# Optimization experiments

Measured on AMD Instinct MI355X. Metric: run time of the kernel, lower is better.

## Reference

```python
import jax, jax.numpy as jnp
import numpy as np
import math

B, S, D_MODEL, H = 4, 256, 2048, 256
HEAD_DIM = D_MODEL // H  # 8


def setup_inputs() -> dict:
    key = jax.random.key(0)
    ks = jax.random.split(key, 10)
    w_scale = 0.02
    inp = {
        "x": jax.random.normal(ks[0], (B, S, D_MODEL), dtype=jnp.float32),
        "phase_shift": jax.random.normal(ks[1], (H, 1, 1), dtype=jnp.float32),
        "Wq": jax.random.normal(ks[2], (D_MODEL, D_MODEL), dtype=jnp.float32) * w_scale,
        "bq": jnp.zeros((D_MODEL,), dtype=jnp.float32),
        "Wk": jax.random.normal(ks[3], (D_MODEL, D_MODEL), dtype=jnp.float32) * w_scale,
        "bk": jnp.zeros((D_MODEL,), dtype=jnp.float32),
        "Wv": jax.random.normal(ks[4], (D_MODEL, D_MODEL), dtype=jnp.float32) * w_scale,
        "bv": jnp.zeros((D_MODEL,), dtype=jnp.float32),
        "Wo": jax.random.normal(ks[5], (D_MODEL, D_MODEL), dtype=jnp.float32) * w_scale,
        "bo": jnp.zeros((D_MODEL,), dtype=jnp.float32),
    }
    return inp


def _forward(x, phase_shift, Wq, bq, Wk, bk, Wv, bv, Wo, bo):
    b, s, dm = x.shape
    h = phase_shift.shape[0]
    d = dm // h
    # projections (torch Linear with random weights; stored as [in,out])
    q = (x @ Wq + bq).reshape(b, s, h, d)
    k = (x @ Wk + bk).reshape(b, s, h, d)
    v = (x @ Wv + bv).reshape(b, s, h, d)
    # complex phase rotation: q *= exp(+i phi), k *= exp(-i phi)
    # phase_shift (h,1,1) broadcasts against (b,s,h,d) -> varies along the s dim (requires s==h)
    c = jnp.cos(phase_shift)  # (h,1,1)
    sn = jnp.sin(phase_shift)
    qr, qi = q * c, q * sn          # Re/Im of rotated q
    kr, ki = k * c, -(k * sn)       # Re/Im of rotated k
    scale = 1.0 / math.sqrt(d)
    # per-(b,s) head-mixing scores: [b,s,h,h], complex matmul split into real/imag
    sr = (jnp.einsum('bshd,bsgd->bshg', qr, kr)
          - jnp.einsum('bshd,bsgd->bshg', qi, ki)) * scale
    si = (jnp.einsum('bshd,bsgd->bshg', qr, ki)
          + jnp.einsum('bshd,bsgd->bshg', qi, kr)) * scale  # analytically 0 (phases cancel)
    attn_r = jax.nn.softmax(sr, axis=-1)
    attn_i = jax.nn.softmax(si, axis=-1)  # faithful dual softmax; v is real so only
    # Re(attention @ v) = attn_r @ v reaches the output (.real is taken before o_proj)
    del attn_i
    out = jnp.einsum('bshg,bsgd->bshd', attn_r, v).reshape(b, s, dm)
    return out @ Wo + bo


def reference(x, phase_shift, Wq, bq, Wk, bk, Wv, bv, Wo, bo):
    return _forward(x, phase_shift, Wq, bq, Wk, bk, Wv, bv, Wo, bo)
```

## Files before the change

### kernel.cpp

```cpp
#include <hip/hip_runtime.h>
#include <math.h>

#define M_TOK 1024
#define DM    2048
#define NH    256
#define HD    8
#define SCALE 0.35355339059327373f
#define LOG2E 1.4426950408889634f

typedef _Float16 f16x8 __attribute__((ext_vector_type(8)));
typedef _Float16 f16x4 __attribute__((ext_vector_type(4)));
typedef float    f32x4 __attribute__((ext_vector_type(4)));

#if defined(__has_builtin)
#  if __has_builtin(__builtin_amdgcn_exp2f)
#    define EXP2(x) __builtin_amdgcn_exp2f(x)
#  endif
#endif
#ifndef EXP2
#  define EXP2(x) exp2f(x)
#endif

template<int N>
__device__ __forceinline__ void vm_wait() {
    if constexpr (N == 0) asm volatile("s_waitcnt vmcnt(0)" ::: "memory");
    else if constexpr (N == 1) asm volatile("s_waitcnt vmcnt(1)" ::: "memory");
    else if constexpr (N == 2) asm volatile("s_waitcnt vmcnt(2)" ::: "memory");
    else if constexpr (N == 3) asm volatile("s_waitcnt vmcnt(3)" ::: "memory");
    else if constexpr (N == 4) asm volatile("s_waitcnt vmcnt(4)" ::: "memory");
    else if constexpr (N == 5) asm volatile("s_waitcnt vmcnt(5)" ::: "memory");
    else if constexpr (N == 6) asm volatile("s_waitcnt vmcnt(6)" ::: "memory");
    else if constexpr (N == 7) asm volatile("s_waitcnt vmcnt(7)" ::: "memory");
    else if constexpr (N == 8) asm volatile("s_waitcnt vmcnt(8)" ::: "memory");
    else static_assert(N <= 8, "add vmcnt case");
}

__device__ __forceinline__ void raw_barrier() {
    asm volatile("" ::: "memory");
    __builtin_amdgcn_s_barrier();
    asm volatile("" ::: "memory");
}

__global__ __launch_bounds__(256) void prep(
    const float* __restrict__ x, _Float16* __restrict__ xh,
    const float* __restrict__ W0, const float* __restrict__ W1,
    const float* __restrict__ W2, const float* __restrict__ W3,
    _Float16* __restrict__ T0, _Float16* __restrict__ T1,
    _Float16* __restrict__ T2, _Float16* __restrict__ T3)
{
    __shared__ float t[64][65];
    const int tid = threadIdx.x;
    const int z   = blockIdx.z;

    if (z == 4) {
        const int i = (blockIdx.y * 32 + blockIdx.x) * 256 + tid;
        const float4 a = ((const float4*)x)[2 * i];
        const float4 b = ((const float4*)x)[2 * i + 1];
        f16x8 v;
        v[0] = (_Float16)a.x; v[1] = (_Float16)a.y; v[2] = (_Float16)a.z; v[3] = (_Float16)a.w;
        v[4] = (_Float16)b.x; v[5] = (_Float16)b.y; v[6] = (_Float16)b.z; v[7] = (_Float16)b.w;
        ((f16x8*)xh)[i] = v;
        return;
    }

    const float* W = (z == 0) ? W0 : (z == 1) ? W1 : (z == 2) ? W2 : W3;
    _Float16*    T = (z == 0) ? T0 : (z == 1) ? T1 : (z == 2) ? T2 : T3;

    const int nb = blockIdx.x * 64;
    const int kb = blockIdx.y * 64;
    const int tr = tid >> 4;
    const int tc = (tid & 15) << 2;

    #pragma unroll
    for (int rr = 0; rr < 4; ++rr) {
        const int k = kb + rr * 16 + tr;
        const float4 v = *(const float4*)&W[(size_t)k * DM + nb + tc];
        t[rr * 16 + tr][tc + 0] = v.x;
        t[rr * 16 + tr][tc + 1] = v.y;
        t[rr * 16 + tr][tc + 2] = v.z;
        t[rr * 16 + tr][tc + 3] = v.w;
    }
    __syncthreads();
    #pragma unroll
    for (int rr = 0; rr < 4; ++rr) {
        const int n = nb + rr * 16 + tr;
        f16x4 v;
        #pragma unroll
        for (int j = 0; j < 4; ++j)
            v[j] = (_Float16)t[tc + j][rr * 16 + tr];
        *(f16x4*)&T[(size_t)n * DM + kb + tc] = v;
    }
}

template<int WGR, int WGC, int WTR, int WTC, bool F16OUT, int MINW, int CS>
__global__ __launch_bounds__(256, MINW) void gemm_db(
    const _Float16* __restrict__ A,
    const _Float16* __restrict__ Bt,
    const float* __restrict__ b0, const float* __restrict__ b1,
    const float* __restrict__ b2, void* __restrict__ C)
{
    constexpr int BM  = WGR * WTR * 16;
    constexpr int BN  = WGC * WTC * 16;
    constexpr int NA  = BM / 8;
    constexpr int NB  = BN / 8;
    constexpr int NC  = NA + NB;
    constexpr int CPW = NC / 4;
    static_assert(NC % 4 == 0);
    constexpr int BUF = (BM + BN) * 64;

    __shared__ _Float16 smem[2 * BUF];

    const int bn = blockIdx.x * BN;
    const int bm = blockIdx.y * BM;

    const int tid  = threadIdx.x;
    const int lane = tid & 63;
    const int wv   = tid >> 6;
    const int wr   = (wv / WGC) * (WTR * 16);
    const int wc   = (wv % WGC) * (WTC * 16);
    const int lr   = lane & 15;
    const int lk   = lane >> 4;
    const int rx   = lr & 7;

    const _Float16* gsrc[CPW];
    int             loff[CPW];
    #pragma unroll
    for (int p = 0; p < CPW; ++p) {
        const int c   = wv * CPW + p;
        const int kch = ((lane & 7) ^ (lane >> 3)) << 3;
        if (c < NA) {
            const int rl = c * 8 + (lane >> 3);
            gsrc[p] = A + (size_t)(bm + rl) * DM + kch;
            loff[p] = c * 512 + lane * 8;
        } else {
            const int rl = (c - NA) * 8 + (lane >> 3);
            gsrc[p] = Bt + (size_t)(bn + rl) * DM + kch;
            loff[p] = BM * 64 + (c - NA) * 512 + lane * 8;
        }
    }

    int offA[WTR][2], offB[WTC][2];
    #pragma unroll
    for (int ks = 0; ks < 2; ++ks) {
        const int sw = (((ks << 2) | lk) ^ rx) << 3;
        #pragma unroll
        for (int i = 0; i < WTR; ++i)
            offA[i][ks] = (wr + i * 16 + lr) * 64 + sw;
        #pragma unroll
        for (int j = 0; j < WTC; ++j)
            offB[j][ks] = BM * 64 + (wc + j * 16 + lr) * 64 + sw;
    }

    f32x4 acc[WTR][WTC] = {};

    auto prefetch = [&](int buf) {
        #pragma unroll
        for (int p = 0; p < CPW; ++p) {
            __builtin_amdgcn_global_load_lds(
                (const __attribute__((address_space(1))) void*)gsrc[p],
                (__attribute__((address_space(3))) void*)(smem + buf * BUF + loff[p]),
                16, 0, 0);
            gsrc[p] += 64;
        }
    };

    auto compute = [&](int buf) {
        const _Float16* base = smem + buf * BUF;
        #pragma unroll
        for (int ks = 0; ks < 2; ++ks) {
            f16x8 aF[WTR], bF[WTC];
            #pragma unroll
            for (int i = 0; i < WTR; ++i)
                aF[i] = *(const f16x8*)&base[offA[i][ks]];
            #pragma unroll
            for (int j = 0; j < WTC; ++j)
                bF[j] = *(const f16x8*)&base[offB[j][ks]];
            __builtin_amdgcn_s_setprio(1);
            #pragma unroll
            for (int i = 0; i < WTR; ++i)
                #pragma unroll
                for (int j = 0; j < WTC; ++j)
                    acc[i][j] = __builtin_amdgcn_mfma_f32_16x16x32_f16(aF[i], bF[j], acc[i][j], 0, 0, 0);
            __builtin_amdgcn_s_setprio(0);
        }
    };

    prefetch(0);
    prefetch(1);
    #pragma unroll 1
    for (int t = 0; t < 32; ++t) {
        if (t < 31) vm_wait<CPW>();
        else        vm_wait<0>();
        raw_barrier();
        compute(t & 1);
        raw_barrier();
        if (t < 30) prefetch(t & 1);
    }

    #pragma unroll
    for (int i = 0; i < WTR; ++i) {
        #pragma unroll
        for (int j = 0; j < WTC; ++j) {
            const int col = bn + wc + j * 16 + lr;
            float bv;
            if constexpr (CS > DM) {
                const float* bp = (col < 2048) ? b0 : (col < 4096) ? b1 : b2;
                bv = bp[col & 2047];
            } else {
                bv = b0[col];
            }
            #pragma unroll
            for (int r = 0; r < 4; ++r) {
                const int row = bm + wr + i * 16 + lk * 4 + r;
                const float v = acc[i][j][r] + bv;
                if (F16OUT)
                    ((_Float16*)C)[(size_t)row * CS + col] = (_Float16)v;
                else
                    ((float*)C)[(size_t)row * CS + col] = v;
            }
        }
    }
}

__global__ __launch_bounds__(256) void attn_mfma(
    const _Float16* __restrict__ QKV, _Float16* __restrict__ Oh)
{
    __shared__ _Float16 Vt[8][264];
    __shared__ _Float16 Al[256][72];
    __shared__ _Float16 Ot[256][8];

    const int tid  = threadIdx.x;
    const int lane = tid & 63;
    const int wv   = tid >> 6;
    const int col  = lane & 15;
    const int quad = lane >> 4;
    const int hbase = wv * 64;

    #pragma unroll 1
    for (int tt = 0; tt < 2; ++tt) {
        const int t = blockIdx.x * 2 + tt;
        const _Float16* qb = QKV + (size_t)t * (3 * DM);
        const _Float16* kb = qb + DM;
        const _Float16* vb = qb + 2 * DM;

        __syncthreads();

        {
            const f16x8 v = *(const f16x8*)(vb + tid * 8);
            #pragma unroll
            for (int d = 0; d < 8; ++d) Vt[d][tid] = v[d];
        }

        f16x8 qf[4];
        #pragma unroll
        for (int ht = 0; ht < 4; ++ht) {
            f16x8 v = {};
            if (quad == 0)
                v = *(const f16x8*)(qb + (hbase + ht * 16 + col) * 8);
            #pragma unroll
            for (int j = 0; j < 8; ++j) qf[ht][j] = v[j] * (_Float16)(SCALE * LOG2E);
        }

        __syncthreads();

        const f32x4 zf = {};
        float rsum[4] = {};
        f32x4 oacc[4] = {};

        #pragma unroll 1
        for (int c = 0; c < 4; ++c) {
            const int gchunk = c * 64;

            f16x8 kf[4];
            #pragma unroll
            for (int gt = 0; gt < 4; ++gt) {
                f16x8 v = {};
                if (quad == 0)
                    v = *(const f16x8*)(kb + (gchunk + gt * 16 + col) * 8);
                kf[gt] = v;
            }

            f32x4 s[4][4];
            #pragma unroll
            for (int gt = 0; gt < 4; ++gt)
                #pragma unroll
                for (int ht = 0; ht < 4; ++ht)
                    s[gt][ht] = __builtin_amdgcn_mfma_f32_16x16x32_f16(kf[gt], qf[ht], zf, 0, 0, 0);

            #pragma unroll
            for (int gt = 0; gt < 4; ++gt) {
                #pragma unroll
                for (int ht = 0; ht < 4; ++ht) {
                    f16x4 e4;
                    #pragma unroll
                    for (int r = 0; r < 4; ++r) {
                        e4[r] = (_Float16)EXP2(s[gt][ht][r]);
                        rsum[ht] += (float)e4[r];
                    }
                    *(f16x4*)&Al[hbase + ht * 16 + col][gt * 16 + quad * 4] = e4;
                }
            }

            #pragma unroll
            for (int ks = 0; ks < 2; ++ks) {
                f16x8 vf = {};
                if (col < 8)
                    vf = *(const f16x8*)&Vt[col][gchunk + ks * 32 + quad * 8];
                #pragma unroll
                for (int ht = 0; ht < 4; ++ht) {
                    const f16x8 af = *(const f16x8*)&Al[hbase + ht * 16 + col][ks * 32 + quad * 8];
                    oacc[ht] = __builtin_amdgcn_mfma_f32_16x16x32_f16(af, vf, oacc[ht], 0, 0, 0);
                }
            }
        }

        #pragma unroll
        for (int ht = 0; ht < 4; ++ht) {
            rsum[ht] += __shfl_xor(rsum[ht], 16, 64);
            rsum[ht] += __shfl_xor(rsum[ht], 32, 64);
        }

        #pragma unroll
        for (int ht = 0; ht < 4; ++ht) {
            #pragma unroll
            for (int r = 0; r < 4; ++r) {
                const float sh = __shfl(rsum[ht], quad * 4 + r, 64);
                const float v  = oacc[ht][r] / sh;
                if (col < 8)
                    Ot[hbase + ht * 16 + quad * 4 + r][col] = (_Float16)v;
            }
        }
        const f16x8 ov = *(const f16x8*)&Ot[tid][0];
        *(f16x8*)(Oh + (size_t)t * DM + tid * 8) = ov;
    }
}

extern "C" void kernel_launch(void* const* d_in, const int* in_sizes, int n_in,
                              void* d_out, int out_size, void* d_ws, size_t ws_size,
                              hipStream_t stream)
{
    const float* x  = (const float*)d_in[0];
    const float* Wq = (const float*)d_in[2];
    const float* bq = (const float*)d_in[3];
    const float* Wk = (const float*)d_in[4];
    const float* bk = (const float*)d_in[5];
    const float* Wv = (const float*)d_in[6];
    const float* bv = (const float*)d_in[7];
    const float* Wo = (const float*)d_in[8];
    const float* bo = (const float*)d_in[9];
    float* out = (float*)d_out;

    char* ws = (char*)d_ws;
    _Float16* xh  = (_Float16*)(ws);
    _Float16* Wt  = (_Float16*)(ws + (4u  << 20));
    _Float16* Wto = (_Float16*)(ws + (28u << 20));
    _Float16* QKV = (_Float16*)(ws + (36u << 20));
    _Float16* Oh  = (_Float16*)(ws + (48u << 20));

    prep<<<dim3(32, 32, 5), dim3(256), 0, stream>>>(
        x, xh, Wq, Wk, Wv, Wo,
        Wt, Wt + 2048 * 2048, Wt + 2 * 2048 * 2048, Wto);

    gemm_db<2, 2, 4, 3, true, 2, 3 * DM><<<dim3(64, 8), dim3(256), 0, stream>>>(
        xh, Wt, bq, bk, bv, (void*)QKV);

    attn_mfma<<<dim3(M_TOK / 2), dim3(256), 0, stream>>>(QKV, Oh);

    gemm_db<1, 4, 2, 2, false, 3, DM><<<dim3(16, 32), dim3(256), 0, stream>>>(
        Oh, Wto, bo, bo, bo, (void*)out);
}
```

Before: 191.7 us.

## Switch GEMMs to 8-wave triple-buffered pipeline with split-phase staging

Replaces the 4-wave double-buffered GEMM with an 8-wave (512-thread) version. It uses three LDS buffers and issues the next-next tile's global-to-LDS loads in two halves interleaved with the two MFMA k-phases. Both projection GEMMs get larger block tiles and half as many blocks, which raises per-block data reuse and keeps more loads in flight. The QKV GEMM now needs roughly 120KB of LDS per block, so only one block fits per CU, and the coarser grid may leave load imbalance across CUs.

```diff
diff --git a/kernel.cpp b/kernel.cpp
--- a/kernel.cpp
+++ b/kernel.cpp
@@ -31,8 +31,7 @@
     else if constexpr (N == 5) asm volatile("s_waitcnt vmcnt(5)" ::: "memory");
     else if constexpr (N == 6) asm volatile("s_waitcnt vmcnt(6)" ::: "memory");
     else if constexpr (N == 7) asm volatile("s_waitcnt vmcnt(7)" ::: "memory");
-    else if constexpr (N == 8) asm volatile("s_waitcnt vmcnt(8)" ::: "memory");
-    else static_assert(N <= 8, "add vmcnt case");
+    else static_assert(N <= 7, "add vmcnt case");
 }
 
 __device__ __forceinline__ void raw_barrier() {
@@ -92,23 +91,28 @@
     }
 }
 
-template<int WGR, int WGC, int WTR, int WTC, bool F16OUT, int MINW, int CS>
-__global__ __launch_bounds__(256, MINW) void gemm_db(
+template<int WGR, int WGC, int WTR, int WTC, bool F16OUT, int CS, bool SPLIT>
+__global__ __launch_bounds__(512, 2) void gemm_p3(
     const _Float16* __restrict__ A,
     const _Float16* __restrict__ Bt,
     const float* __restrict__ b0, const float* __restrict__ b1,
     const float* __restrict__ b2, void* __restrict__ C)
 {
+    constexpr int NW  = WGR * WGC;
+    static_assert(NW == 8, "8 waves");
     constexpr int BM  = WGR * WTR * 16;
     constexpr int BN  = WGC * WTC * 16;
     constexpr int NA  = BM / 8;
     constexpr int NB  = BN / 8;
     constexpr int NC  = NA + NB;
-    constexpr int CPW = NC / 4;
-    static_assert(NC % 4 == 0);
+    constexpr int CPW = NC / NW;
+    static_assert(NC % NW == 0);
+    constexpr int S0  = (CPW + 1) / 2;
     constexpr int BUF = (BM + BN) * 64;
-
-    __shared__ _Float16 smem[2 * BUF];
+    constexpr int KT  = 32;
+    static_assert((KT - 2) % 3 == 0 || true);
+
+    __shared__ _Float16 smem[3 * BUF];
 
     const int bn = blockIdx.x * BN;
     const int bm = blockIdx.y * BM;
@@ -153,49 +157,60 @@
 
     f32x4 acc[WTR][WTC] = {};
 
-    auto prefetch = [&](int buf) {
+    auto stage = [&](int buf, int from, int to) {
         #pragma unroll
         for (int p = 0; p < CPW; ++p) {
-            __builtin_amdgcn_global_load_lds(
-                (const __attribute__((address_space(1))) void*)gsrc[p],
-                (__attribute__((address_space(3))) void*)(smem + buf * BUF + loff[p]),
-                16, 0, 0);
-            gsrc[p] += 64;
+            if (p >= from && p < to) {
+                __builtin_amdgcn_global_load_lds(
+                    (const __attribute__((address_space(1))) void*)gsrc[p],
+                    (__attribute__((address_space(3))) void*)(smem + buf * BUF + loff[p]),
+                    16, 0, 0);
+                gsrc[p] += 64;
+            }
         }
     };
 
-    auto compute = [&](int buf) {
+    auto cphase = [&](int buf, int ks) {
         const _Float16* base = smem + buf * BUF;
-        #pragma unroll
-        for (int ks = 0; ks < 2; ++ks) {
-            f16x8 aF[WTR], bF[WTC];
-            #pragma unroll
-            for (int i = 0; i < WTR; ++i)
-                aF[i] = *(const f16x8*)&base[offA[i][ks]];
+        f16x8 aF[WTR], bF[WTC];
+        #pragma unroll
+        for (int i = 0; i < WTR; ++i)
+            aF[i] = *(const f16x8*)&base[offA[i][ks]];
+        #pragma unroll
+        for (int j = 0; j < WTC; ++j)
+            bF[j] = *(const f16x8*)&base[offB[j][ks]];
+        __builtin_amdgcn_s_setprio(1);
+        #pragma unroll
+        for (int i = 0; i < WTR; ++i)
             #pragma unroll
             for (int j = 0; j < WTC; ++j)
-                bF[j] = *(const f16x8*)&base[offB[j][ks]];
-            __builtin_amdgcn_s_setprio(1);
-            #pragma unroll
-            for (int i = 0; i < WTR; ++i)
-                #pragma unroll
-                for (int j = 0; j < WTC; ++j)
-                    acc[i][j] = __builtin_amdgcn_mfma_f32_16x16x32_f16(aF[i], bF[j], acc[i][j], 0, 0, 0);
-            __builtin_amdgcn_s_setprio(0);
-        }
+                acc[i][j] = __builtin_amdgcn_mfma_f32_16x16x32_f16(aF[i], bF[j], acc[i][j], 0, 0, 0);
+        __builtin_amdgcn_s_setprio(0);
     };
 
-    prefetch(0);
-    prefetch(1);
+    auto tile = [&](int buf, bool do_stage, bool last) {
+        if (last) vm_wait<0>();
+        else      vm_wait<CPW>();
+        raw_barrier();
+        const int nb3 = (buf + 2 >= 3) ? buf - 1 : buf + 2;
+        if (do_stage) stage(nb3, 0, S0);
+        cphase(buf, 0);
+        if (SPLIT) raw_barrier();
+        if (do_stage) stage(nb3, S0, CPW);
+        cphase(buf, 1);
+        raw_barrier();
+    };
+
+    stage(0, 0, CPW);
+    stage(1, 0, CPW);
     #pragma unroll 1
-    for (int t = 0; t < 32; ++t) {
-        if (t < 31) vm_wait<CPW>();
-        else        vm_wait<0>();
-        raw_barrier();
-        compute(t & 1);
-        raw_barrier();
-        if (t < 30) prefetch(t & 1);
-    }
+    for (int tt = 0; tt < KT - 2; tt += 3) {
+        tile(0, true, false);
+        tile(1, true, false);
+        tile(2, true, false);
+    }
+    tile(0, false, false);
+    tile(1, false, true);
 
     #pragma unroll
     for (int i = 0; i < WTR; ++i) {
@@ -361,11 +376,11 @@
         x, xh, Wq, Wk, Wv, Wo,
         Wt, Wt + 2048 * 2048, Wt + 2 * 2048 * 2048, Wto);
 
-    gemm_db<2, 2, 4, 3, true, 2, 3 * DM><<<dim3(64, 8), dim3(256), 0, stream>>>(
+    gemm_p3<2, 4, 4, 3, true, 3 * DM, true><<<dim3(32, 8), dim3(512), 0, stream>>>(
         xh, Wt, bq, bk, bv, (void*)QKV);
 
     attn_mfma<<<dim3(M_TOK / 2), dim3(256), 0, stream>>>(QKV, Oh);
 
-    gemm_db<1, 4, 2, 2, false, 3, DM><<<dim3(16, 32), dim3(256), 0, stream>>>(
+    gemm_p3<2, 4, 2, 2, false, DM, false><<<dim3(16, 16), dim3(512), 0, stream>>>(
         Oh, Wto, bo, bo, bo, (void*)out);
 }
```

New measurement: 185.2 us. 3.4% less time.
